# Kernel optimization log

Hardware: AMD Instinct MI355X
Metric: run time of the kernel (lower is better)

The kernel has to match this reference:

```python
import jax, jax.numpy as jnp
import numpy as np
from jax import lax

B, L, H = 2, 1024, 1024
D = 2048          # intermediate_size
N = 16            # ssm state size
K = 4             # conv kernel
R = 64            # time_step_rank


def setup_inputs() -> dict:
    key = jax.random.key(0)
    ks = jax.random.split(key, 10)
    def nrm(k, shape, scale=0.02):
        return jax.random.normal(k, shape, dtype=jnp.float32) * scale
    A = jnp.arange(1, N + 1, dtype=jnp.float32)[None, :] * jnp.ones((D, 1), jnp.float32)
    return {
        "hidden_states": jax.random.normal(ks[0], (B, L, H), dtype=jnp.float32),
        "W_in":  nrm(ks[1], (2 * D, H)),
        "conv_w": nrm(ks[2], (D, 1, K), 0.1),
        "conv_b": nrm(ks[3], (D,), 0.1),
        "W_x":   nrm(ks[4], (R + 2 * N, D)),
        "W_dt":  nrm(ks[5], (D, R), 0.1),
        "b_dt":  jnp.full((D,), -4.6, jnp.float32),  # softplus(-4.6) ~ 0.01 dt init
        "A_log": jnp.log(A),
        "D_param": jnp.ones((D,), jnp.float32),
        "W_out": nrm(ks[6], (H, D)),
    }


def _mamba_forward(hidden_states, W_in, conv_w, conv_b, W_x, W_dt, b_dt, A_log, D_param, W_out):
    silu = jax.nn.silu
    # in_proj -> [B, L, 2D], chunk into x and gate
    proj = jnp.einsum("blh,eh->ble", hidden_states, W_in)
    x, gate = jnp.split(proj, 2, axis=-1)           # [B,L,D] each
    # depthwise causal conv over time: [B,D,L]
    xc = x.swapaxes(1, 2)
    xc = lax.conv_general_dilated(
        xc, conv_w, window_strides=(1,), padding=[(K - 1, 0)],
        dimension_numbers=("NCH", "OIH", "NCH"), feature_group_count=D)
    x = silu(xc + conv_b[None, :, None]).swapaxes(1, 2)   # [B,L,D]
    # x_proj -> dt, Bmat, Cmat
    ssm_p = jnp.einsum("bld,rd->blr", x, W_x)             # [B,L,R+2N]
    dt_lr, Bm, Cm = ssm_p[..., :R], ssm_p[..., R:R + N], ssm_p[..., R + N:]
    dt = jax.nn.softplus(jnp.einsum("blr,dr->bld", dt_lr, W_dt) + b_dt)  # [B,L,D]
    A = -jnp.exp(A_log)                                   # [D,N]
    dA = jnp.exp(dt[..., None] * A[None, None])           # [B,L,D,N]
    dBu = dt[..., None] * Bm[:, :, None, :] * x[..., None]  # [B,L,D,N]
    # selective scan over time
    def step(h, inp):
        dA_t, dBu_t, C_t = inp                            # [B,D,N],[B,D,N],[B,N]
        h = dA_t * h + dBu_t
        y = jnp.einsum("bdn,bn->bd", h, C_t)
        return h, y
    h0 = jnp.zeros((B, D, N), dt.dtype)
    _, ys = lax.scan(step, h0, (dA.swapaxes(0, 1), dBu.swapaxes(0, 1), Cm.swapaxes(0, 1)))
    y = ys.swapaxes(0, 1)                                 # [B,L,D]
    y = (y + x * D_param[None, None, :]) * silu(gate)
    return jnp.einsum("bld,hd->blh", y, W_out)            # [B,L,H]


def reference(hidden_states, W_in, conv_w, conv_b, W_x, W_dt, b_dt, A_log, D_param, W_out):
    return _mamba_forward(hidden_states, W_in, conv_w, conv_b, W_x, W_dt, b_dt, A_log, D_param, W_out)
```

## Files before the change

kernel.cpp:

```cpp
#include <hip/hip_runtime.h>
#include <hip/hip_bf16.h>
#include <math.h>

#define B_ 2
#define L_ 1024
#define H_ 1024
#define D_ 2048
#define N_ 16
#define R_ 64
#define NCK 32
#define CL 32

typedef short short8 __attribute__((ext_vector_type(8)));
typedef float floatx4 __attribute__((ext_vector_type(4)));

__device__ __forceinline__ float siluf(float g) {
    return g / (1.0f + __expf(-g));
}

__device__ __forceinline__ unsigned short f2bf(float f) {
    unsigned int u = __float_as_uint(f);
    u = (u + 0x7fffu + ((u >> 16) & 1u)) >> 16;
    return (unsigned short)u;
}

__device__ __forceinline__ float bf2f(unsigned short u) {
    return __uint_as_float(((unsigned int)u) << 16);
}

__device__ __forceinline__ void gl2lds(const unsigned short* g, unsigned short* l) {
    __builtin_amdgcn_global_load_lds(
        (const __attribute__((address_space(1))) unsigned int*)g,
        (__attribute__((address_space(3))) unsigned int*)l, 16, 0, 0);
}

#define Q0 524288
#define Q1 1572864
#define Q2 2097152
#define Q3 2146304
#define Q4 2179072
__global__ __launch_bounds__(256) void cvt_all(
    const float* __restrict__ i0, const float* __restrict__ i1,
    const float* __restrict__ i2, const float* __restrict__ i3,
    const float* __restrict__ i4,
    unsigned short* __restrict__ o0, unsigned short* __restrict__ o1,
    unsigned short* __restrict__ o2, unsigned short* __restrict__ o3,
    unsigned short* __restrict__ o4)
{
    int q = blockIdx.x * 256 + threadIdx.x;
    if (q >= Q4) return;
    const float* in; unsigned short* out; int base;
    if (q < Q0)      { in = i0; out = o0; base = 0; }
    else if (q < Q1) { in = i1; out = o1; base = Q0; }
    else if (q < Q2) { in = i2; out = o2; base = Q1; }
    else if (q < Q3) { in = i3; out = o3; base = Q2; }
    else             { in = i4; out = o4; base = Q3; }
    int i = (q - base) * 4;
    float4 v = *(const float4*)(in + i);
    ushort4 o;
    o.x = f2bf(v.x); o.y = f2bf(v.y); o.z = f2bf(v.z); o.w = f2bf(v.w);
    *(ushort4*)(out + i) = o;
}

template<int EPI>
__global__ __launch_bounds__(256) void gemm128(
    const unsigned short* __restrict__ A, const unsigned short* __restrict__ Bm,
    float* __restrict__ C, int K, int ldc, int kChunk,
    size_t partStride, float* __restrict__ C2)
{
    __shared__ unsigned short As[2][128 * 64];
    __shared__ unsigned short Bs[2][128 * 64];
    const int tid  = threadIdx.x;
    const int lane = tid & 63;
    const int wave = tid >> 6;
    const int wm = (wave >> 1) * 64;
    const int wn = (wave & 1) * 64;
    const int lr   = lane & 15;
    const int quad = lane >> 4;

    const int nwg = gridDim.x * gridDim.y * gridDim.z;
    const int lin = blockIdx.x + gridDim.x * (blockIdx.y + gridDim.y * blockIdx.z);
    const int swz = (lin & 7) * (nwg >> 3) + (lin >> 3);
    const int bx  = swz % gridDim.x;
    const int tmp = swz / gridDim.x;
    const int by  = tmp % gridDim.y;
    const int bz  = tmp / gridDim.y;

    const int m0 = by * 128;
    const int n0 = bx * 128;
    const int k0 = bz * kChunk;

    const int rowIn8 = lane >> 3;
    const int colSw  = ((lane & 7) ^ rowIn8) * 8;
    const int srow   = wave * 8 + rowIn8;
    const size_t aoff0 = (size_t)(m0 + srow +  0) * K + colSw;
    const size_t aoff1 = (size_t)(m0 + srow + 32) * K + colSw;
    const size_t aoff2 = (size_t)(m0 + srow + 64) * K + colSw;
    const size_t aoff3 = (size_t)(m0 + srow + 96) * K + colSw;
    const size_t boff0 = (size_t)(n0 + srow +  0) * K + colSw;
    const size_t boff1 = (size_t)(n0 + srow + 32) * K + colSw;
    const size_t boff2 = (size_t)(n0 + srow + 64) * K + colSw;
    const size_t boff3 = (size_t)(n0 + srow + 96) * K + colSw;
    const int rq0 = ((quad) ^ (lr & 7)) * 8;
    const int rq1 = rq0 ^ 32;

    floatx4 acc[4][4];
#pragma unroll
    for (int mi = 0; mi < 4; ++mi)
#pragma unroll
        for (int ni = 0; ni < 4; ++ni)
            acc[mi][ni] = (floatx4){0.f, 0.f, 0.f, 0.f};

#define STG(buf, kt)                                                    \
    do {                                                                \
        gl2lds(A + aoff0 + (kt), &As[buf][(0  + wave * 8) * 64]);       \
        gl2lds(A + aoff1 + (kt), &As[buf][(32 + wave * 8) * 64]);       \
        gl2lds(A + aoff2 + (kt), &As[buf][(64 + wave * 8) * 64]);       \
        gl2lds(A + aoff3 + (kt), &As[buf][(96 + wave * 8) * 64]);       \
        gl2lds(Bm + boff0 + (kt), &Bs[buf][(0  + wave * 8) * 64]);      \
        gl2lds(Bm + boff1 + (kt), &Bs[buf][(32 + wave * 8) * 64]);      \
        gl2lds(Bm + boff2 + (kt), &Bs[buf][(64 + wave * 8) * 64]);      \
        gl2lds(Bm + boff3 + (kt), &Bs[buf][(96 + wave * 8) * 64]);      \
    } while (0)

    STG(0, k0);

    const int nt = kChunk >> 6;
    for (int t = 0; t < nt; ++t) {
        const int cur = t & 1;
        if (t + 1 < nt) {
            STG(cur ^ 1, k0 + (t + 1) * 64);
            asm volatile("s_waitcnt vmcnt(8)" ::: "memory");
        } else {
            asm volatile("s_waitcnt vmcnt(0)" ::: "memory");
        }
        __builtin_amdgcn_s_barrier();
        __builtin_amdgcn_sched_barrier(0);

        short8 a0f[4], a1f[4], b0f[4], b1f[4];
#pragma unroll
        for (int mi = 0; mi < 4; ++mi) {
            a0f[mi] = *(const short8*)&As[cur][(wm + mi * 16 + lr) * 64 + rq0];
            a1f[mi] = *(const short8*)&As[cur][(wm + mi * 16 + lr) * 64 + rq1];
        }
#pragma unroll
        for (int ni = 0; ni < 4; ++ni) {
            b0f[ni] = *(const short8*)&Bs[cur][(wn + ni * 16 + lr) * 64 + rq0];
            b1f[ni] = *(const short8*)&Bs[cur][(wn + ni * 16 + lr) * 64 + rq1];
        }
#pragma unroll
        for (int mi = 0; mi < 4; ++mi)
#pragma unroll
            for (int ni = 0; ni < 4; ++ni)
                acc[mi][ni] = __builtin_amdgcn_mfma_f32_16x16x32_bf16(
                    a0f[mi], b0f[ni], acc[mi][ni], 0, 0, 0);
#pragma unroll
        for (int mi = 0; mi < 4; ++mi)
#pragma unroll
            for (int ni = 0; ni < 4; ++ni)
                acc[mi][ni] = __builtin_amdgcn_mfma_f32_16x16x32_bf16(
                    a1f[mi], b1f[ni], acc[mi][ni], 0, 0, 0);

        asm volatile("s_waitcnt lgkmcnt(0)" ::: "memory");
        __builtin_amdgcn_s_barrier();
    }
#undef STG

    float* Cz = C + (size_t)bz * partStride;
#pragma unroll
    for (int mi = 0; mi < 4; ++mi)
#pragma unroll
        for (int ni = 0; ni < 4; ++ni) {
            const int rr = m0 + wm + mi * 16 + quad * 4;
            const int cc = n0 + wn + ni * 16 + lr;
            if (EPI == 4) {
                if (cc < 2048) {
#pragma unroll
                    for (int r = 0; r < 4; ++r)
                        C[(size_t)(rr + r) * 2048 + cc] = acc[mi][ni][r];
                } else {
#pragma unroll
                    for (int r = 0; r < 4; ++r)
                        C2[(size_t)(rr + r) * 2048 + (cc - 2048)] = acc[mi][ni][r];
                }
            } else {
#pragma unroll
                for (int r = 0; r < 4; ++r)
                    Cz[(size_t)(rr + r) * ldc + cc] = acc[mi][ni][r];
            }
        }
}

__global__ __launch_bounds__(256) void gemm_ssm(
    const unsigned short* __restrict__ A, const unsigned short* __restrict__ Bm,
    float* __restrict__ C, int K, int Ncols, int ldc, int kChunk, int nMax,
    size_t partStride)
{
    __shared__ unsigned short As[2][64 * 64];
    __shared__ unsigned short Bs[2][128 * 64];
    const int tid  = threadIdx.x;
    const int lane = tid & 63;
    const int wave = tid >> 6;
    const int wm = (wave >> 1) * 32;
    const int wn = (wave & 1) * 64;
    const int lr   = lane & 15;
    const int quad = lane >> 4;
    const int m0 = blockIdx.y * 64;
    const int n0 = blockIdx.x * 128;
    const int k0 = blockIdx.z * kChunk;

    const int rowIn8 = lane >> 3;
    const int colSw  = ((lane & 7) ^ rowIn8) * 8;
    const size_t aoff0 = (size_t)(m0 + 0  + wave * 8 + rowIn8) * K + colSw;
    const size_t aoff1 = (size_t)(m0 + 32 + wave * 8 + rowIn8) * K + colSw;
    const size_t boff0 = (size_t)min(n0 + 0  + wave * 8 + rowIn8, nMax - 1) * K + colSw;
    const size_t boff1 = (size_t)min(n0 + 32 + wave * 8 + rowIn8, nMax - 1) * K + colSw;
    const size_t boff2 = (size_t)min(n0 + 64 + wave * 8 + rowIn8, nMax - 1) * K + colSw;
    const size_t boff3 = (size_t)min(n0 + 96 + wave * 8 + rowIn8, nMax - 1) * K + colSw;
    const int rq0 = ((quad) ^ (lr & 7)) * 8;
    const int rq1 = rq0 ^ 32;

    floatx4 acc[2][4];
#pragma unroll
    for (int mi = 0; mi < 2; ++mi)
#pragma unroll
        for (int ni = 0; ni < 4; ++ni)
            acc[mi][ni] = (floatx4){0.f, 0.f, 0.f, 0.f};

#define STAGE(buf, kt)                                                   \
    do {                                                                 \
        gl2lds(A + aoff0 + (kt), &As[buf][(0  + wave * 8) * 64]);        \
        gl2lds(A + aoff1 + (kt), &As[buf][(32 + wave * 8) * 64]);        \
        gl2lds(Bm + boff0 + (kt), &Bs[buf][(0   + wave * 8) * 64]);      \
        gl2lds(Bm + boff1 + (kt), &Bs[buf][(32  + wave * 8) * 64]);      \
        gl2lds(Bm + boff2 + (kt), &Bs[buf][(64  + wave * 8) * 64]);      \
        gl2lds(Bm + boff3 + (kt), &Bs[buf][(96  + wave * 8) * 64]);      \
    } while (0)

    STAGE(0, k0);

    const int nt = kChunk >> 6;
    for (int t = 0; t < nt; ++t) {
        const int cur = t & 1;
        if (t + 1 < nt) {
            STAGE(cur ^ 1, k0 + (t + 1) * 64);
            asm volatile("s_waitcnt vmcnt(6)" ::: "memory");
        } else {
            asm volatile("s_waitcnt vmcnt(0)" ::: "memory");
        }
        __builtin_amdgcn_s_barrier();
        __builtin_amdgcn_sched_barrier(0);

        short8 a0[2], a1[2], b0[4], b1[4];
#pragma unroll
        for (int mi = 0; mi < 2; ++mi) {
            a0[mi] = *(const short8*)&As[cur][(wm + mi * 16 + lr) * 64 + rq0];
            a1[mi] = *(const short8*)&As[cur][(wm + mi * 16 + lr) * 64 + rq1];
        }
#pragma unroll
        for (int ni = 0; ni < 4; ++ni) {
            b0[ni] = *(const short8*)&Bs[cur][(wn + ni * 16 + lr) * 64 + rq0];
            b1[ni] = *(const short8*)&Bs[cur][(wn + ni * 16 + lr) * 64 + rq1];
        }
#pragma unroll
        for (int mi = 0; mi < 2; ++mi)
#pragma unroll
            for (int ni = 0; ni < 4; ++ni)
                acc[mi][ni] = __builtin_amdgcn_mfma_f32_16x16x32_bf16(
                    a0[mi], b0[ni], acc[mi][ni], 0, 0, 0);
#pragma unroll
        for (int mi = 0; mi < 2; ++mi)
#pragma unroll
            for (int ni = 0; ni < 4; ++ni)
                acc[mi][ni] = __builtin_amdgcn_mfma_f32_16x16x32_bf16(
                    a1[mi], b1[ni], acc[mi][ni], 0, 0, 0);

        asm volatile("s_waitcnt lgkmcnt(0)" ::: "memory");
        __builtin_amdgcn_s_barrier();
    }
#undef STAGE

    float* Cz = C + (size_t)blockIdx.z * partStride;
#pragma unroll
    for (int mi = 0; mi < 2; ++mi)
#pragma unroll
        for (int ni = 0; ni < 4; ++ni) {
            const int rr = m0 + wm + mi * 16 + quad * 4;
            const int cc = n0 + wn + ni * 16 + lr;
            if (cc >= Ncols) continue;
#pragma unroll
            for (int r = 0; r < 4; ++r)
                Cz[(size_t)(rr + r) * ldc + cc] = acc[mi][ni][r];
        }
}

__global__ __launch_bounds__(256) void reduce_ssm(
    const float* __restrict__ P, float* __restrict__ ssm_p,
    unsigned short* __restrict__ sp64)
{
    const int q = blockIdx.x * 256 + threadIdx.x;
    const int m = q / 24;
    const int c = (q - m * 24) * 4;
    const size_t idx = (size_t)m * 96 + c;
    float4 s = make_float4(0.f, 0.f, 0.f, 0.f);
#pragma unroll
    for (int z = 0; z < 16; ++z) {
        float4 v = *(const float4*)(P + (size_t)z * (2048 * 96) + idx);
        s.x += v.x; s.y += v.y; s.z += v.z; s.w += v.w;
    }
    *(float4*)(ssm_p + idx) = s;
    if (c < 64) {
        ushort4 o;
        o.x = f2bf(s.x); o.y = f2bf(s.y); o.z = f2bf(s.z); o.w = f2bf(s.w);
        *(ushort4*)(sp64 + (size_t)m * 64 + c) = o;
    }
}

__global__ __launch_bounds__(256) void reduce_out(
    const float* __restrict__ P, float* __restrict__ out)
{
    const size_t i = ((size_t)blockIdx.x * 256 + threadIdx.x) * 4;
    float4 a = *(const float4*)(P + i);
    float4 b = *(const float4*)(P + 2097152 + i);
    float4 c = *(const float4*)(P + 2 * 2097152 + i);
    float4 d = *(const float4*)(P + 3 * 2097152 + i);
    *(float4*)(out + i) = make_float4(a.x + b.x + c.x + d.x,
                                      a.y + b.y + c.y + d.y,
                                      a.z + b.z + c.z + d.z,
                                      a.w + b.w + c.w + d.w);
}

__global__ __launch_bounds__(256) void dt_gemm(
    const unsigned short* __restrict__ A,
    const unsigned short* __restrict__ Bm,
    float* __restrict__ C,
    const float* __restrict__ bias)
{
    __shared__ unsigned short As[64 * 72];
    __shared__ unsigned short Bs[64 * 72];
    const int tid = threadIdx.x;
    const int lane = tid & 63;
    const int wave = tid >> 6;
    const int lr = lane & 15;
    const int quad = lane >> 4;
    const int n0 = blockIdx.x * 64;
    const int m0 = blockIdx.y * 64;

    {
        const int row = tid >> 3;
        const int cq = (tid & 7) * 8;
        uint4 a0 = *(const uint4*)(A + (size_t)(m0 + row) * 64 + cq);
        uint4 a1 = *(const uint4*)(A + (size_t)(m0 + 32 + row) * 64 + cq);
        uint4 b0 = *(const uint4*)(Bm + (size_t)(n0 + row) * 64 + cq);
        uint4 b1 = *(const uint4*)(Bm + (size_t)(n0 + 32 + row) * 64 + cq);
        *(uint4*)&As[row * 72 + cq] = a0;
        *(uint4*)&As[(32 + row) * 72 + cq] = a1;
        *(uint4*)&Bs[row * 72 + cq] = b0;
        *(uint4*)&Bs[(32 + row) * 72 + cq] = b1;
    }
    __syncthreads();

    floatx4 acc[4];
#pragma unroll
    for (int ni = 0; ni < 4; ++ni) acc[ni] = (floatx4){0.f, 0.f, 0.f, 0.f};

#pragma unroll
    for (int kt = 0; kt < 64; kt += 32) {
        short8 af = *(const short8*)&As[(wave * 16 + lr) * 72 + kt + quad * 8];
#pragma unroll
        for (int ni = 0; ni < 4; ++ni) {
            short8 bf = *(const short8*)&Bs[(ni * 16 + lr) * 72 + kt + quad * 8];
            acc[ni] = __builtin_amdgcn_mfma_f32_16x16x32_bf16(af, bf, acc[ni], 0, 0, 0);
        }
    }

    const int rr = m0 + wave * 16 + quad * 4;
#pragma unroll
    for (int ni = 0; ni < 4; ++ni) {
        const int cc = n0 + ni * 16 + lr;
        const float bv = bias[cc];
#pragma unroll
        for (int r = 0; r < 4; ++r) {
            const float z = acc[ni][r] + bv;
            const float spv = fmaxf(z, 0.f) + __logf(1.f + __expf(-fabsf(z)));
            C[(size_t)(rr + r) * 2048 + cc] = spv;
        }
    }
}

__global__ __launch_bounds__(256) void conv_silu_kernel(
    const float* __restrict__ xpre, const float* __restrict__ conv_w,
    const float* __restrict__ conv_b, unsigned short* __restrict__ x_bf)
{
    __shared__ float inT[67][64];
    __shared__ unsigned short tile[64][72];
    const int t = threadIdx.x;
    const int d0 = blockIdx.x * 64;
    const int lt0 = blockIdx.y * 64;
    const int b = blockIdx.z;

    {
        const int r = t >> 2;
        const int q = (t & 3) * 16;
        const int l = lt0 + r - 3;
        if (l >= 0) {
            const float* src = xpre + ((size_t)(b * 1024 + l)) * 2048 + d0 + q;
            *(float4*)&inT[r][q + 0]  = *(const float4*)(src + 0);
            *(float4*)&inT[r][q + 4]  = *(const float4*)(src + 4);
            *(float4*)&inT[r][q + 8]  = *(const float4*)(src + 8);
            *(float4*)&inT[r][q + 12] = *(const float4*)(src + 12);
        } else {
            float4 z4 = make_float4(0.f, 0.f, 0.f, 0.f);
            *(float4*)&inT[r][q + 0]  = z4;
            *(float4*)&inT[r][q + 4]  = z4;
            *(float4*)&inT[r][q + 8]  = z4;
            *(float4*)&inT[r][q + 12] = z4;
        }
        if (t < 12) {
            const int r2 = 64 + (t >> 2);
            const int l2 = lt0 + r2 - 3;
            const float* src = xpre + ((size_t)(b * 1024 + l2)) * 2048 + d0 + q;
            *(float4*)&inT[r2][q + 0]  = *(const float4*)(src + 0);
            *(float4*)&inT[r2][q + 4]  = *(const float4*)(src + 4);
            *(float4*)&inT[r2][q + 8]  = *(const float4*)(src + 8);
            *(float4*)&inT[r2][q + 12] = *(const float4*)(src + 12);
        }
    }
    __syncthreads();

    const int dl = t & 63;
    const int seg = t >> 6;
    const int d = d0 + dl;
    const float w0 = conv_w[d * 4 + 0], w1 = conv_w[d * 4 + 1];
    const float w2 = conv_w[d * 4 + 2], w3 = conv_w[d * 4 + 3];
    const float bias = conv_b[d];

    float p[19];
#pragma unroll
    for (int j = 0; j < 19; ++j) p[j] = inT[seg * 16 + j][dl];
#pragma unroll
    for (int j = 0; j < 16; ++j) {
        float v = siluf(bias + w0 * p[j] + w1 * p[j + 1] + w2 * p[j + 2] + w3 * p[j + 3]);
        tile[seg * 16 + j][dl] = f2bf(v);
    }
    __syncthreads();

    const int ml = t >> 2;
    const int c = t & 3;
    short8 s0 = *(const short8*)&tile[ml][c * 16];
    short8 s1 = *(const short8*)&tile[ml][c * 16 + 8];
    unsigned short* dst = x_bf + (size_t)(b * 1024 + lt0 + ml) * 2048 + d0 + c * 16;
    *(short8*)dst = s0;
    *(short8*)(dst + 8) = s1;
}

__global__ __launch_bounds__(256) void scan_p1(
    const float* __restrict__ dt, const unsigned short* __restrict__ x_bf,
    const float* __restrict__ sp, const float* __restrict__ A_log,
    float* __restrict__ Dts, float* __restrict__ Hch)
{
    __shared__ float sB[CL][16];
    const int tid = threadIdx.x;
    const int d = blockIdx.x * 256 + tid;
    const int ck = blockIdx.y;
    const int b = blockIdx.z;
    const int mb = b * 1024 + ck * CL;

    if (tid < CL * 4) {
        int row = tid >> 2, q = (tid & 3) * 4;
        *(float4*)&sB[row][q] = *(const float4*)(sp + (size_t)(mb + row) * 96 + 64 + q);
    }
    float An2[16];
    {
        const float* al = A_log + d * 16;
#pragma unroll
        for (int j = 0; j < 16; j += 4) {
            float4 a4 = *(const float4*)(al + j);
            An2[j + 0] = -__expf(a4.x) * 1.44269504f;
            An2[j + 1] = -__expf(a4.y) * 1.44269504f;
            An2[j + 2] = -__expf(a4.z) * 1.44269504f;
            An2[j + 3] = -__expf(a4.w) * 1.44269504f;
        }
    }
    __syncthreads();

    float h[16];
#pragma unroll
    for (int n = 0; n < 16; ++n) h[n] = 0.f;
    float dts = 0.f;

    for (int l = 0; l < CL; ++l) {
        const size_t off = (size_t)(mb + l) * 2048 + d;
        const float dtv = dt[off];
        const float xv = bf2f(x_bf[off]);
        const float u = dtv * xv;
        dts += dtv;
        float4 B0 = *(const float4*)&sB[l][0];
        float4 B1 = *(const float4*)&sB[l][4];
        float4 B2 = *(const float4*)&sB[l][8];
        float4 B3 = *(const float4*)&sB[l][12];
        float Bv[16] = {B0.x, B0.y, B0.z, B0.w, B1.x, B1.y, B1.z, B1.w,
                        B2.x, B2.y, B2.z, B2.w, B3.x, B3.y, B3.z, B3.w};
#pragma unroll
        for (int n = 0; n < 16; ++n) {
            const float dA = __builtin_amdgcn_exp2f(dtv * An2[n]);
            h[n] = fmaf(dA, h[n], Bv[n] * u);
        }
    }

    const size_t cb = (size_t)(b * NCK + ck) * 2048 + d;
    Dts[cb] = dts;
    const size_t base = cb * 16;
#pragma unroll
    for (int j = 0; j < 16; j += 4)
        *(float4*)(Hch + base + j) = make_float4(h[j], h[j + 1], h[j + 2], h[j + 3]);
}

__global__ __launch_bounds__(256) void scan_combine(
    const float* __restrict__ Dts, const float* __restrict__ Hch,
    const float* __restrict__ A_log, float* __restrict__ Hin)
{
    const int flat = blockIdx.x * 256 + threadIdx.x;
    const int dn = flat & 32767;
    const int b = flat >> 15;
    const int d = dn >> 4;
    const float An2 = -__expf(A_log[dn]) * 1.44269504f;
    float hin = 0.f;
#pragma unroll 4
    for (int ck = 0; ck < NCK; ++ck) {
        const size_t cb = (size_t)(b * NCK + ck) * 2048 + d;
        const float p = __builtin_amdgcn_exp2f(Dts[cb] * An2);
        const size_t a = ((size_t)(b * NCK + ck) << 15) + dn;
        const float hc = Hch[a];
        Hin[a] = hin;
        hin = fmaf(p, hin, hc);
    }
}

__global__ __launch_bounds__(256) void scan_p2(
    const float* __restrict__ dt, const unsigned short* __restrict__ x_bf,
    const float* __restrict__ gate, const float* __restrict__ sp,
    const float* __restrict__ A_log, const float* __restrict__ Dp,
    const float* __restrict__ Hin, unsigned short* __restrict__ y_bf)
{
    __shared__ float sBC[CL][32];
    const int tid = threadIdx.x;
    const int d = blockIdx.x * 256 + tid;
    const int ck = blockIdx.y;
    const int b = blockIdx.z;
    const int mb = b * 1024 + ck * CL;

    {
        int row = tid >> 3, q = (tid & 7) * 4;
        *(float4*)&sBC[row][q] = *(const float4*)(sp + (size_t)(mb + row) * 96 + 64 + q);
    }
    float An2[16];
    {
        const float* al = A_log + d * 16;
#pragma unroll
        for (int j = 0; j < 16; j += 4) {
            float4 a4 = *(const float4*)(al + j);
            An2[j + 0] = -__expf(a4.x) * 1.44269504f;
            An2[j + 1] = -__expf(a4.y) * 1.44269504f;
            An2[j + 2] = -__expf(a4.z) * 1.44269504f;
            An2[j + 3] = -__expf(a4.w) * 1.44269504f;
        }
    }
    float h[16];
    {
        const size_t base = ((size_t)(b * NCK + ck) * 2048 + d) * 16;
#pragma unroll
        for (int j = 0; j < 16; j += 4) {
            float4 hv = *(const float4*)(Hin + base + j);
            h[j] = hv.x; h[j + 1] = hv.y; h[j + 2] = hv.z; h[j + 3] = hv.w;
        }
    }
    const float Dv = Dp[d];
    __syncthreads();

    for (int l = 0; l < CL; ++l) {
        const size_t off = (size_t)(mb + l) * 2048 + d;
        const float dtv = dt[off];
        const float xv = bf2f(x_bf[off]);
        const float gv = gate[off];
        const float u = dtv * xv;
        float4 B0 = *(const float4*)&sBC[l][0];
        float4 B1 = *(const float4*)&sBC[l][4];
        float4 B2 = *(const float4*)&sBC[l][8];
        float4 B3 = *(const float4*)&sBC[l][12];
        float Bv[16] = {B0.x, B0.y, B0.z, B0.w, B1.x, B1.y, B1.z, B1.w,
                        B2.x, B2.y, B2.z, B2.w, B3.x, B3.y, B3.z, B3.w};
#pragma unroll
        for (int n = 0; n < 16; ++n) {
            const float dA = __builtin_amdgcn_exp2f(dtv * An2[n]);
            h[n] = fmaf(dA, h[n], Bv[n] * u);
        }
        float4 C0 = *(const float4*)&sBC[l][16];
        float4 C1 = *(const float4*)&sBC[l][20];
        float4 C2 = *(const float4*)&sBC[l][24];
        float4 C3 = *(const float4*)&sBC[l][28];
        float Cv[16] = {C0.x, C0.y, C0.z, C0.w, C1.x, C1.y, C1.z, C1.w,
                        C2.x, C2.y, C2.z, C2.w, C3.x, C3.y, C3.z, C3.w};
        float p = 0.f;
#pragma unroll
        for (int n = 0; n < 16; ++n)
            p = fmaf(h[n], Cv[n], p);
        y_bf[off] = f2bf(fmaf(xv, Dv, p) * siluf(gv));
    }
}

extern "C" void kernel_launch(void* const* d_in, const int* in_sizes, int n_in,
                              void* d_out, int out_size, void* d_ws, size_t ws_size,
                              hipStream_t stream)
{
    const float* hs     = (const float*)d_in[0];
    const float* W_in   = (const float*)d_in[1];
    const float* conv_w = (const float*)d_in[2];
    const float* conv_b = (const float*)d_in[3];
    const float* W_x    = (const float*)d_in[4];
    const float* W_dt   = (const float*)d_in[5];
    const float* b_dt   = (const float*)d_in[6];
    const float* A_log  = (const float*)d_in[7];
    const float* Dp     = (const float*)d_in[8];
    const float* W_out  = (const float*)d_in[9];
    float* out = (float*)d_out;

    float* ws    = (float*)d_ws;
    float* gate  = ws;
    float* dtb   = gate + (size_t)4194304;
    float* xpre  = dtb + (size_t)4194304;
    float* ssm_p = xpre + (size_t)4194304;
    unsigned short* hs_bf    = (unsigned short*)(ssm_p + 196608);
    unsigned short* W_in_bf  = hs_bf + (size_t)2097152;
    unsigned short* W_out_bf = W_in_bf + (size_t)4194304;
    unsigned short* W_x_bf   = W_out_bf + (size_t)2097152;
    unsigned short* W_dt_bf  = W_x_bf + (size_t)196608;
    unsigned short* sp64_bf  = W_dt_bf + (size_t)131072;
    unsigned short* x_bf     = sp64_bf + (size_t)131072;
    float* Dts  = (float*)(x_bf + (size_t)4194304);
    float* P1   = xpre;
    float* Hin  = xpre;
    float* Hch  = xpre + (size_t)2097152;
    float* Pout = gate;
    unsigned short* y_bf = hs_bf;

    const int M = B_ * L_;

    cvt_all<<<(Q4 + 255) / 256, 256, 0, stream>>>(
        hs, W_in, W_out, W_x, W_dt, hs_bf, W_in_bf, W_out_bf, W_x_bf, W_dt_bf);

    gemm128<4><<<dim3(4096 / 128, M / 128, 1), 256, 0, stream>>>(
        hs_bf, W_in_bf, xpre, 1024, 2048, 1024, 0, gate);

    conv_silu_kernel<<<dim3(D_ / 64, L_ / 64, B_), 256, 0, stream>>>(
        xpre, conv_w, conv_b, x_bf);

    gemm_ssm<<<dim3(1, M / 64, 16), 256, 0, stream>>>(
        x_bf, W_x_bf, P1, 2048, 96, 96, 128, 96, (size_t)2048 * 96);

    reduce_ssm<<<(2048 * 24) / 256, 256, 0, stream>>>(P1, ssm_p, sp64_bf);

    dt_gemm<<<dim3(2048 / 64, 2048 / 64), 256, 0, stream>>>(
        sp64_bf, W_dt_bf, dtb, b_dt);

    scan_p1<<<dim3(D_ / 256, NCK, B_), 256, 0, stream>>>(
        dtb, x_bf, ssm_p, A_log, Dts, Hch);
    scan_combine<<<(B_ * D_ * 16) / 256, 256, 0, stream>>>(Dts, Hch, A_log, Hin);
    scan_p2<<<dim3(D_ / 256, NCK, B_), 256, 0, stream>>>(
        dtb, x_bf, gate, ssm_p, A_log, Dp, Hin, y_bf);

    gemm128<0><<<dim3(1024 / 128, M / 128, 4), 256, 0, stream>>>(
        y_bf, W_out_bf, Pout, 2048, 1024, 512, (size_t)2048 * 1024, nullptr);

    reduce_out<<<(2048 * 1024 / 4) / 256, 256, 0, stream>>>(Pout, out);
}
```

Before: 220.0 us.

## Fuse dt projection GEMM and softplus into both scan passes

Removes the standalone dt_gemm kernel and recomputes each chunk's dt tile (32 timesteps x 256 channels) with MFMA inside scan_p1 and scan_p2, storing it in shared memory. This avoids writing and twice re-reading a 2048x2048 fp32 dt tensor in global memory and saves one launch. In exchange the small GEMM and the softplus are computed twice, and each scan block uses more LDS, which may lower occupancy.

```diff
diff --git a/kernel.cpp b/kernel.cpp
--- a/kernel.cpp
+++ b/kernel.cpp
@@ -328,64 +328,6 @@
                                       a.y + b.y + c.y + d.y,
                                       a.z + b.z + c.z + d.z,
                                       a.w + b.w + c.w + d.w);
-}
-
-__global__ __launch_bounds__(256) void dt_gemm(
-    const unsigned short* __restrict__ A,
-    const unsigned short* __restrict__ Bm,
-    float* __restrict__ C,
-    const float* __restrict__ bias)
-{
-    __shared__ unsigned short As[64 * 72];
-    __shared__ unsigned short Bs[64 * 72];
-    const int tid = threadIdx.x;
-    const int lane = tid & 63;
-    const int wave = tid >> 6;
-    const int lr = lane & 15;
-    const int quad = lane >> 4;
-    const int n0 = blockIdx.x * 64;
-    const int m0 = blockIdx.y * 64;
-
-    {
-        const int row = tid >> 3;
-        const int cq = (tid & 7) * 8;
-        uint4 a0 = *(const uint4*)(A + (size_t)(m0 + row) * 64 + cq);
-        uint4 a1 = *(const uint4*)(A + (size_t)(m0 + 32 + row) * 64 + cq);
-        uint4 b0 = *(const uint4*)(Bm + (size_t)(n0 + row) * 64 + cq);
-        uint4 b1 = *(const uint4*)(Bm + (size_t)(n0 + 32 + row) * 64 + cq);
-        *(uint4*)&As[row * 72 + cq] = a0;
-        *(uint4*)&As[(32 + row) * 72 + cq] = a1;
-        *(uint4*)&Bs[row * 72 + cq] = b0;
-        *(uint4*)&Bs[(32 + row) * 72 + cq] = b1;
-    }
-    __syncthreads();
-
-    floatx4 acc[4];
-#pragma unroll
-    for (int ni = 0; ni < 4; ++ni) acc[ni] = (floatx4){0.f, 0.f, 0.f, 0.f};
-
-#pragma unroll
-    for (int kt = 0; kt < 64; kt += 32) {
-        short8 af = *(const short8*)&As[(wave * 16 + lr) * 72 + kt + quad * 8];
-#pragma unroll
-        for (int ni = 0; ni < 4; ++ni) {
-            short8 bf = *(const short8*)&Bs[(ni * 16 + lr) * 72 + kt + quad * 8];
-            acc[ni] = __builtin_amdgcn_mfma_f32_16x16x32_bf16(af, bf, acc[ni], 0, 0, 0);
-        }
-    }
-
-    const int rr = m0 + wave * 16 + quad * 4;
-#pragma unroll
-    for (int ni = 0; ni < 4; ++ni) {
-        const int cc = n0 + ni * 16 + lr;
-        const float bv = bias[cc];
-#pragma unroll
-        for (int r = 0; r < 4; ++r) {
-            const float z = acc[ni][r] + bv;
-            const float spv = fmaxf(z, 0.f) + __logf(1.f + __expf(-fabsf(z)));
-            C[(size_t)(rr + r) * 2048 + cc] = spv;
-        }
-    }
 }
 
 __global__ __launch_bounds__(256) void conv_silu_kernel(
@@ -454,17 +396,72 @@
     *(short8*)(dst + 8) = s1;
 }
 
+__device__ __forceinline__ void dt_tile(
+    const unsigned short* __restrict__ sp64,
+    const unsigned short* __restrict__ Wdt,
+    const float* __restrict__ bias,
+    int mb, int d0, int lane, int wave, int lr, int quad,
+    float (*dtile)[260])
+{
+    floatx4 acc[2][4];
+#pragma unroll
+    for (int mi = 0; mi < 2; ++mi)
+#pragma unroll
+        for (int ni = 0; ni < 4; ++ni)
+            acc[mi][ni] = (floatx4){0.f, 0.f, 0.f, 0.f};
+
+#pragma unroll
+    for (int s = 0; s < 2; ++s) {
+        short8 af[2], bf[4];
+#pragma unroll
+        for (int mi = 0; mi < 2; ++mi)
+            af[mi] = *(const short8*)&sp64[(size_t)(mb + mi * 16 + lr) * 64 + s * 32 + quad * 8];
+#pragma unroll
+        for (int ni = 0; ni < 4; ++ni)
+            bf[ni] = *(const short8*)&Wdt[(size_t)(d0 + wave * 64 + ni * 16 + lr) * 64 + s * 32 + quad * 8];
+#pragma unroll
+        for (int mi = 0; mi < 2; ++mi)
+#pragma unroll
+            for (int ni = 0; ni < 4; ++ni)
+                acc[mi][ni] = __builtin_amdgcn_mfma_f32_16x16x32_bf16(
+                    af[mi], bf[ni], acc[mi][ni], 0, 0, 0);
+    }
+
+#pragma unroll
+    for (int ni = 0; ni < 4; ++ni) {
+        const int cc = wave * 64 + ni * 16 + lr;
+        const float bv = bias[d0 + cc];
+#pragma unroll
+        for (int mi = 0; mi < 2; ++mi)
+#pragma unroll
+            for (int r = 0; r < 4; ++r) {
+                const float z = acc[mi][ni][r] + bv;
+                const float spv = fmaxf(z, 0.f) + __logf(1.f + __expf(-fabsf(z)));
+                dtile[mi * 16 + quad * 4 + r][cc] = spv;
+            }
+    }
+}
+
 __global__ __launch_bounds__(256) void scan_p1(
-    const float* __restrict__ dt, const unsigned short* __restrict__ x_bf,
+    const unsigned short* __restrict__ sp64, const unsigned short* __restrict__ Wdt,
+    const float* __restrict__ b_dt, const unsigned short* __restrict__ x_bf,
     const float* __restrict__ sp, const float* __restrict__ A_log,
     float* __restrict__ Dts, float* __restrict__ Hch)
 {
     __shared__ float sB[CL][16];
+    __shared__ float dtile[CL][260];
     const int tid = threadIdx.x;
-    const int d = blockIdx.x * 256 + tid;
+    const int lane = tid & 63;
+    const int wave = tid >> 6;
+    const int lr = lane & 15;
+    const int quad = lane >> 4;
+    const int d0 = blockIdx.x * 256;
+    const int d = d0 + tid;
     const int ck = blockIdx.y;
     const int b = blockIdx.z;
     const int mb = b * 1024 + ck * CL;
+
+    dt_tile(sp64, Wdt, b_dt, mb, d0, lane, wave, lr, quad, dtile);
 
     if (tid < CL * 4) {
         int row = tid >> 2, q = (tid & 3) * 4;
@@ -491,7 +488,7 @@
 
     for (int l = 0; l < CL; ++l) {
         const size_t off = (size_t)(mb + l) * 2048 + d;
-        const float dtv = dt[off];
+        const float dtv = dtile[l][tid];
         const float xv = bf2f(x_bf[off]);
         const float u = dtv * xv;
         dts += dtv;
@@ -538,17 +535,26 @@
 }
 
 __global__ __launch_bounds__(256) void scan_p2(
-    const float* __restrict__ dt, const unsigned short* __restrict__ x_bf,
+    const unsigned short* __restrict__ sp64, const unsigned short* __restrict__ Wdt,
+    const float* __restrict__ b_dt, const unsigned short* __restrict__ x_bf,
     const float* __restrict__ gate, const float* __restrict__ sp,
     const float* __restrict__ A_log, const float* __restrict__ Dp,
     const float* __restrict__ Hin, unsigned short* __restrict__ y_bf)
 {
     __shared__ float sBC[CL][32];
+    __shared__ float dtile[CL][260];
     const int tid = threadIdx.x;
-    const int d = blockIdx.x * 256 + tid;
+    const int lane = tid & 63;
+    const int wave = tid >> 6;
+    const int lr = lane & 15;
+    const int quad = lane >> 4;
+    const int d0 = blockIdx.x * 256;
+    const int d = d0 + tid;
     const int ck = blockIdx.y;
     const int b = blockIdx.z;
     const int mb = b * 1024 + ck * CL;
+
+    dt_tile(sp64, Wdt, b_dt, mb, d0, lane, wave, lr, quad, dtile);
 
     {
         int row = tid >> 3, q = (tid & 7) * 4;
@@ -580,7 +586,7 @@
 
     for (int l = 0; l < CL; ++l) {
         const size_t off = (size_t)(mb + l) * 2048 + d;
-        const float dtv = dt[off];
+        const float dtv = dtile[l][tid];
         const float xv = bf2f(x_bf[off]);
         const float gv = gate[off];
         const float u = dtv * xv;
@@ -660,14 +666,11 @@
 
     reduce_ssm<<<(2048 * 24) / 256, 256, 0, stream>>>(P1, ssm_p, sp64_bf);
 
-    dt_gemm<<<dim3(2048 / 64, 2048 / 64), 256, 0, stream>>>(
-        sp64_bf, W_dt_bf, dtb, b_dt);
-
     scan_p1<<<dim3(D_ / 256, NCK, B_), 256, 0, stream>>>(
-        dtb, x_bf, ssm_p, A_log, Dts, Hch);
+        sp64_bf, W_dt_bf, b_dt, x_bf, ssm_p, A_log, Dts, Hch);
     scan_combine<<<(B_ * D_ * 16) / 256, 256, 0, stream>>>(Dts, Hch, A_log, Hin);
     scan_p2<<<dim3(D_ / 256, NCK, B_), 256, 0, stream>>>(
-        dtb, x_bf, gate, ssm_p, A_log, Dp, Hin, y_bf);
+        sp64_bf, W_dt_bf, b_dt, x_bf, gate, ssm_p, A_log, Dp, Hin, y_bf);
 
     gemm128<0><<<dim3(1024 / 128, M / 128, 4), 256, 0, stream>>>(
         y_bf, W_out_bf, Pout, 2048, 1024, 512, (size_t)2048 * 1024, nullptr);
```

Result: faster. 211.1 us (median of 2 runs) (-4.1%).
